# Performance work log

Hardware: AMD Instinct MI355X
Metric: run time of the kernel (lower is better)

## Reference

```python
import jax, jax.numpy as jnp
import numpy as np

# gcn_module: out[b] = (adj[b] @ x[b].T).T  <=>  out[b, d, n] = sum_m adj[b, n, m] * x[b, d, m]
# The torch code loops over the batch with per-sample torch.mm; here it is a single batched einsum.

def setup_inputs() -> dict:
    key = jax.random.key(0)
    k1, k2 = jax.random.split(key)
    B, D, N = 2, 3072, 8192  # D = 48*8*8 unfold features, N = (1024/8)*(512/8) patches
    x = jax.random.normal(k1, (B, D, N), dtype=jnp.float32)
    adj = jax.random.normal(k2, (B, N, N), dtype=jnp.float32)
    return {"x": x, "adj": adj}


def reference(x, adj):
    # [B, D, N] = einsum over neighbor axis m of the (dense) graph-laplacian adjacency
    return jnp.einsum('bnm,bdm->bdn', adj, x)
```

## Files before the change

### kernel.cpp

```cpp
#include <hip/hip_runtime.h>
#include <stdint.h>

#define GM 3072
#define GN 8192
#define GK 8192
#define GB 2

#define BM 128
#define BN 128
#define BK 64

typedef __bf16 bf16x8 __attribute__((ext_vector_type(8)));
typedef float f32x4 __attribute__((ext_vector_type(4)));
typedef unsigned short u16x8 __attribute__((ext_vector_type(8)));

__device__ __forceinline__ unsigned short f2bf(float f) {
  union { float f; unsigned u; } v; v.f = f;
  return (unsigned short)((v.u + 0x7FFFu + ((v.u >> 16) & 1u)) >> 16);
}

__device__ __forceinline__ void gl2lds16(const void* g, void* l) {
  __builtin_amdgcn_global_load_lds(
      (const __attribute__((address_space(1))) unsigned int*)g,
      (__attribute__((address_space(3))) unsigned int*)l, 16, 0, 0);
}

__global__ void cvt_f32_bf16(const float4* __restrict__ in,
                             ushort4* __restrict__ out, int n4) {
  int i = blockIdx.x * blockDim.x + threadIdx.x;
  int stride = gridDim.x * blockDim.x;
  for (; i < n4; i += stride) {
    float4 f = in[i];
    ushort4 o;
    o.x = f2bf(f.x); o.y = f2bf(f.y); o.z = f2bf(f.z); o.w = f2bf(f.w);
    out[i] = o;
  }
}

template <bool ASYNC>
__global__ __launch_bounds__(256) void gcn_gemm(const void* __restrict__ Av,
                                                const void* __restrict__ Bv,
                                                float* __restrict__ C) {
  __shared__ __attribute__((aligned(16))) uint16_t sA[BM * BK];
  __shared__ __attribute__((aligned(16))) uint16_t sB[BN * BK];

  const int tid = threadIdx.x;
  const int lane = tid & 63;
  const int w = tid >> 6;
  const int wm = w >> 1;
  const int wn = w & 1;
  const int t16 = lane & 15;
  const int q = lane >> 4;

  const int b = blockIdx.z;
  const int m0 = blockIdx.y * BM;
  const int n0 = blockIdx.x * BN;

  f32x4 acc[4][4] = {};
  const int swz = t16 & 7;

  for (int k0 = 0; k0 < GK; k0 += BK) {
    if (ASYNC) {
      const uint16_t* Ab = (const uint16_t*)Av + (size_t)b * GM * GK + (size_t)m0 * GK + k0;
      const uint16_t* Bb = (const uint16_t*)Bv + (size_t)b * GN * GK + (size_t)n0 * GK + k0;
#pragma unroll
      for (int i = 0; i < 4; i++) {
        const int t = i * 256 + tid;
        const int row = t >> 3;
        const int segg = (t & 7) ^ (row & 7);
        gl2lds16(Ab + (size_t)row * GK + segg * 8,
                 (char*)sA + (size_t)(i * 256 + w * 64) * 16);
        gl2lds16(Bb + (size_t)row * GK + segg * 8,
                 (char*)sB + (size_t)(i * 256 + w * 64) * 16);
      }
    } else {
      const float* Af = (const float*)Av + (size_t)b * GM * GK + (size_t)m0 * GK + k0;
      const float* Bf = (const float*)Bv + (size_t)b * GN * GK + (size_t)n0 * GK + k0;
#pragma unroll
      for (int i = 0; i < 4; i++) {
        const int t = i * 256 + tid;
        const int row = t >> 3;
        const int segg = (t & 7) ^ (row & 7);
        {
          const float* p = Af + (size_t)row * GK + segg * 8;
          float4 f0 = *(const float4*)p;
          float4 f1 = *(const float4*)(p + 4);
          u16x8 vv = {f2bf(f0.x), f2bf(f0.y), f2bf(f0.z), f2bf(f0.w),
                      f2bf(f1.x), f2bf(f1.y), f2bf(f1.z), f2bf(f1.w)};
          *(u16x8*)((char*)sA + (size_t)t * 16) = vv;
        }
        {
          const float* p = Bf + (size_t)row * GK + segg * 8;
          float4 f0 = *(const float4*)p;
          float4 f1 = *(const float4*)(p + 4);
          u16x8 vv = {f2bf(f0.x), f2bf(f0.y), f2bf(f0.z), f2bf(f0.w),
                      f2bf(f1.x), f2bf(f1.y), f2bf(f1.z), f2bf(f1.w)};
          *(u16x8*)((char*)sB + (size_t)t * 16) = vv;
        }
      }
    }
    __syncthreads();

#pragma unroll
    for (int s = 0; s < BK / 32; s++) {
      bf16x8 af[4], bfr[4];
#pragma unroll
      for (int i = 0; i < 4; i++) {
        const int r = wm * 64 + i * 16 + t16;
        af[i] = *(const bf16x8*)((const char*)sA + r * (BK * 2) +
                                 (((s * 4 + q) ^ swz) * 16));
      }
#pragma unroll
      for (int j = 0; j < 4; j++) {
        const int r = wn * 64 + j * 16 + t16;
        bfr[j] = *(const bf16x8*)((const char*)sB + r * (BK * 2) +
                                  (((s * 4 + q) ^ swz) * 16));
      }
#pragma unroll
      for (int i = 0; i < 4; i++)
#pragma unroll
        for (int j = 0; j < 4; j++)
          acc[i][j] = __builtin_amdgcn_mfma_f32_16x16x32_bf16(af[i], bfr[j],
                                                              acc[i][j], 0, 0, 0);
    }
    __syncthreads();
  }

  float* Cp = C + (size_t)b * GM * GN;
#pragma unroll
  for (int i = 0; i < 4; i++) {
    const int rowb = m0 + wm * 64 + i * 16 + q * 4;
#pragma unroll
    for (int j = 0; j < 4; j++) {
      const int col = n0 + wn * 64 + j * 16 + t16;
#pragma unroll
      for (int r = 0; r < 4; r++)
        Cp[(size_t)(rowb + r) * GN + col] = acc[i][j][r];
    }
  }
}

extern "C" void kernel_launch(void* const* d_in, const int* in_sizes, int n_in,
                              void* d_out, int out_size, void* d_ws, size_t ws_size,
                              hipStream_t stream) {
  const float* x = (const float*)d_in[0];
  const float* adj = (const float*)d_in[1];
  float* out = (float*)d_out;

  const size_t xe = (size_t)GB * GM * GK;
  const size_t ae = (size_t)GB * GN * GK;
  const size_t need = (xe + ae) * sizeof(uint16_t);

  dim3 grid(GN / BN, GM / BM, GB);

  if (ws_size >= need) {
    uint16_t* xb = (uint16_t*)d_ws;
    uint16_t* ab = xb + xe;
    cvt_f32_bf16<<<4096, 256, 0, stream>>>((const float4*)x, (ushort4*)xb, (int)(xe / 4));
    cvt_f32_bf16<<<4096, 256, 0, stream>>>((const float4*)adj, (ushort4*)ab, (int)(ae / 4));
    gcn_gemm<true><<<grid, 256, 0, stream>>>(xb, ab, out);
  } else {
    gcn_gemm<false><<<grid, 256, 0, stream>>>(x, adj, out);
  }
}
```

Before: 1.908 ms.

## Add 256x256 double-buffered pipelined bf16 GEMM kernel with 8 waves

Replaces the 128x128 single-buffered async GEMM with a 256x256-tile kernel using 512 threads, two LDS buffers split into half-K sub-tiles, and a phased schedule. Each phase issues the global-to-LDS loads for a future tile while the MFMAs on the current tile run, using explicit vmcnt waits, barriers and setprio. The goal is to hide global load latency and raise data reuse per tile. In exchange it needs more registers and LDS per block, which limits occupancy, and the hand-tuned wait counts are fragile.

```diff
diff --git a/kernel.cpp b/kernel.cpp
--- a/kernel.cpp
+++ b/kernel.cpp
@@ -5,10 +5,6 @@
 #define GN 8192
 #define GK 8192
 #define GB 2
-
-#define BM 128
-#define BN 128
-#define BK 64
 
 typedef __bf16 bf16x8 __attribute__((ext_vector_type(8)));
 typedef float f32x4 __attribute__((ext_vector_type(4)));
@@ -37,6 +33,10 @@
   }
 }
 
+#define BM 128
+#define BN 128
+#define BK 64
+
 template <bool ASYNC>
 __global__ __launch_bounds__(256) void gcn_gemm(const void* __restrict__ Av,
                                                 const void* __restrict__ Bv,
@@ -60,20 +60,7 @@
   const int swz = t16 & 7;
 
   for (int k0 = 0; k0 < GK; k0 += BK) {
-    if (ASYNC) {
-      const uint16_t* Ab = (const uint16_t*)Av + (size_t)b * GM * GK + (size_t)m0 * GK + k0;
-      const uint16_t* Bb = (const uint16_t*)Bv + (size_t)b * GN * GK + (size_t)n0 * GK + k0;
-#pragma unroll
-      for (int i = 0; i < 4; i++) {
-        const int t = i * 256 + tid;
-        const int row = t >> 3;
-        const int segg = (t & 7) ^ (row & 7);
-        gl2lds16(Ab + (size_t)row * GK + segg * 8,
-                 (char*)sA + (size_t)(i * 256 + w * 64) * 16);
-        gl2lds16(Bb + (size_t)row * GK + segg * 8,
-                 (char*)sB + (size_t)(i * 256 + w * 64) * 16);
-      }
-    } else {
+    {
       const float* Af = (const float*)Av + (size_t)b * GM * GK + (size_t)m0 * GK + k0;
       const float* Bf = (const float*)Bv + (size_t)b * GN * GK + (size_t)n0 * GK + k0;
 #pragma unroll
@@ -140,6 +127,127 @@
   }
 }
 
+#define CBM 256
+#define CBN 256
+#define CBK 64
+#define NTILES (GK / CBK)
+#define NITER (NTILES / 2)
+
+#define STAGE(Base, kt, kh, dstp)                                              \
+  do {                                                                         \
+    const uint16_t* src_ = (Base) + (size_t)(kt) * CBK + (kh) * 32;            \
+    _Pragma("unroll") for (int si_ = 0; si_ < 2; si_++) {                      \
+      const int t_ = si_ * 512 + tid;                                          \
+      const int row_ = t_ >> 2;                                                \
+      const int qs_ = (t_ & 3) ^ ((row_ >> 1) & 3);                            \
+      gl2lds16(src_ + (size_t)row_ * GK + qs_ * 8,                             \
+               (char*)(dstp) + ((si_ * 512 + (tid & ~63)) * 16));              \
+    }                                                                          \
+  } while (0)
+
+#define VM6 asm volatile("s_waitcnt vmcnt(6)" ::: "memory")
+#define VM0 asm volatile("s_waitcnt vmcnt(0)" ::: "memory")
+#define NOVM ((void)0)
+#define NOST ((void)0)
+
+#define PHASE(c, s, h, STAGES, VM)                                             \
+  do {                                                                         \
+    const char* Ar_ = (const char*)&smem[c][0][s][0];                          \
+    const char* Br_ = (const char*)&smem[c][1][s][0];                          \
+    if ((h) == 0) {                                                            \
+      _Pragma("unroll") for (int j_ = 0; j_ < 4; j_++)                         \
+          bfr[j_] = *(const bf16x8*)(Br_ + (wn * 64 + j_ * 16 + t16) * 64 + qp); \
+    }                                                                          \
+    _Pragma("unroll") for (int fi_ = 0; fi_ < 4; fi_++)                        \
+        af[fi_] = *(const bf16x8*)(Ar_ + (wm * 128 + (h) * 64 + fi_ * 16 + t16) * 64 + qp); \
+    STAGES;                                                                    \
+    VM;                                                                        \
+    __builtin_amdgcn_sched_barrier(0);                                         \
+    __builtin_amdgcn_s_barrier();                                              \
+    asm volatile("s_waitcnt lgkmcnt(0)" ::: "memory");                         \
+    __builtin_amdgcn_sched_barrier(0);                                         \
+    __builtin_amdgcn_s_setprio(1);                                             \
+    _Pragma("unroll") for (int fi_ = 0; fi_ < 4; fi_++)                        \
+        _Pragma("unroll") for (int j_ = 0; j_ < 4; j_++)                       \
+            acc[(h) * 4 + fi_][j_] = __builtin_amdgcn_mfma_f32_16x16x32_bf16(  \
+                af[fi_], bfr[j_], acc[(h) * 4 + fi_][j_], 0, 0, 0);            \
+    __builtin_amdgcn_s_setprio(0);                                             \
+    __builtin_amdgcn_sched_barrier(0);                                         \
+    __builtin_amdgcn_s_barrier();                                              \
+  } while (0)
+
+__global__ __launch_bounds__(512, 2) void gcn_gemm256(
+    const uint16_t* __restrict__ A, const uint16_t* __restrict__ B,
+    float* __restrict__ C) {
+  __shared__ __attribute__((aligned(16))) uint16_t smem[2][2][2][256 * 32];
+
+  const int tid = threadIdx.x;
+  const int lane = tid & 63;
+  const int w = tid >> 6;
+  const int wm = w >> 2;
+  const int wn = w & 3;
+  const int t16 = lane & 15;
+  const int q = lane >> 4;
+  const int qp = (q ^ ((t16 >> 1) & 3)) << 4;
+
+  const int b = blockIdx.z;
+  const int m0 = blockIdx.y * CBM;
+  const int n0 = blockIdx.x * CBN;
+
+  const uint16_t* Ab = A + (size_t)b * GM * GK + (size_t)m0 * GK;
+  const uint16_t* Bb = B + (size_t)b * GN * GK + (size_t)n0 * GK;
+
+  f32x4 acc[8][4] = {};
+  bf16x8 af[4], bfr[4];
+
+  STAGE(Ab, 0, 0, &smem[0][0][0][0]);
+  STAGE(Ab, 0, 1, &smem[0][0][1][0]);
+  STAGE(Bb, 0, 0, &smem[0][1][0][0]);
+  STAGE(Bb, 0, 1, &smem[0][1][1][0]);
+  STAGE(Bb, 1, 0, &smem[1][1][0][0]);
+  STAGE(Ab, 1, 0, &smem[1][0][0][0]);
+  STAGE(Bb, 1, 1, &smem[1][1][1][0]);
+  VM6;
+  __builtin_amdgcn_sched_barrier(0);
+  __builtin_amdgcn_s_barrier();
+
+  for (int it = 0; it < NITER - 1; ++it) {
+    const int tO = 2 * it + 1;
+    const int tE2 = 2 * it + 2;
+    const int tO2 = 2 * it + 3;
+    PHASE(0, 0, 0, STAGE(Ab, tO, 1, &smem[1][0][1][0]), NOVM);
+    PHASE(0, 0, 1, STAGE(Bb, tE2, 0, &smem[0][1][0][0]), NOVM);
+    PHASE(0, 1, 0, STAGE(Ab, tE2, 0, &smem[0][0][0][0]), NOVM);
+    PHASE(0, 1, 1, STAGE(Bb, tE2, 1, &smem[0][1][1][0]), VM6);
+    PHASE(1, 0, 0, STAGE(Ab, tE2, 1, &smem[0][0][1][0]), NOVM);
+    PHASE(1, 0, 1, STAGE(Bb, tO2, 0, &smem[1][1][0][0]), NOVM);
+    PHASE(1, 1, 0, STAGE(Ab, tO2, 0, &smem[1][0][0][0]), NOVM);
+    PHASE(1, 1, 1, STAGE(Bb, tO2, 1, &smem[1][1][1][0]), VM6);
+  }
+
+  PHASE(0, 0, 0, STAGE(Ab, NTILES - 1, 1, &smem[1][0][1][0]), NOVM);
+  PHASE(0, 0, 1, NOST, NOVM);
+  PHASE(0, 1, 0, NOST, NOVM);
+  PHASE(0, 1, 1, NOST, VM0);
+  PHASE(1, 0, 0, NOST, NOVM);
+  PHASE(1, 0, 1, NOST, NOVM);
+  PHASE(1, 1, 0, NOST, NOVM);
+  PHASE(1, 1, 1, NOST, NOVM);
+
+  float* Cp = C + (size_t)b * GM * GN;
+#pragma unroll
+  for (int i = 0; i < 8; i++) {
+    const int rowb = m0 + wm * 128 + i * 16 + q * 4;
+#pragma unroll
+    for (int j = 0; j < 4; j++) {
+      const int col = n0 + wn * 64 + j * 16 + t16;
+#pragma unroll
+      for (int r = 0; r < 4; r++)
+        Cp[(size_t)(rowb + r) * GN + col] = acc[i][j][r];
+    }
+  }
+}
+
 extern "C" void kernel_launch(void* const* d_in, const int* in_sizes, int n_in,
                               void* d_out, int out_size, void* d_ws, size_t ws_size,
                               hipStream_t stream) {
@@ -151,15 +259,15 @@
   const size_t ae = (size_t)GB * GN * GK;
   const size_t need = (xe + ae) * sizeof(uint16_t);
 
-  dim3 grid(GN / BN, GM / BM, GB);
-
   if (ws_size >= need) {
     uint16_t* xb = (uint16_t*)d_ws;
     uint16_t* ab = xb + xe;
     cvt_f32_bf16<<<4096, 256, 0, stream>>>((const float4*)x, (ushort4*)xb, (int)(xe / 4));
     cvt_f32_bf16<<<4096, 256, 0, stream>>>((const float4*)adj, (ushort4*)ab, (int)(ae / 4));
-    gcn_gemm<true><<<grid, 256, 0, stream>>>(xb, ab, out);
+    dim3 grid(GN / CBN, GM / CBM, GB);
+    gcn_gemm256<<<grid, 512, 0, stream>>>(xb, ab, out);
   } else {
+    dim3 grid(GN / BN, GM / BM, GB);
     gcn_gemm<false><<<grid, 256, 0, stream>>>(x, adj, out);
   }
 }
```

New measurement: 1.535 ms. 1.24x faster.
